# Performance work log

Measured on AMD Instinct MI355X. Metric: run time of the kernel, lower is better.

## Reference

```python
import jax, jax.numpy as jnp
import numpy as np

B, CD, ZL = 512, 64, 16
HID, SE, NC, SL = 512, 512, 9, 64
EPS = 1e-5


def _conv_t1d(x, w, b, stride, opad):
    # torch ConvTranspose1d weight layout: [in, out, k]; pad=0
    k = w.shape[-1]
    w2 = jnp.flip(jnp.transpose(w, (1, 0, 2)), -1)  # [out, in, k]
    y = jax.lax.conv_general_dilated(
        x, w2, window_strides=(1,),
        padding=[(k - 1, k - 1 + opad)], lhs_dilation=(stride,),
        dimension_numbers=('NCH', 'OIH', 'NCH'))
    return y + b[None, :, None]


def _bn(x, g, bt, m, v):  # eval-mode BatchNorm1d over channel dim of [B,C,L]
    return (x - m[None, :, None]) * (g * jax.lax.rsqrt(v + EPS))[None, :, None] + bt[None, :, None]


def _gru(x, h, wih, whh, bih, bhh):  # torch GRUCell gate order r,z,n
    gi = x @ wih.T + bih
    gh = h @ whh.T + bhh
    ir, iz, inn = jnp.split(gi, 3, axis=-1)
    hr, hz, hn = jnp.split(gh, 3, axis=-1)
    r = jax.nn.sigmoid(ir + hr)
    z = jax.nn.sigmoid(iz + hz)
    n = jnp.tanh(inn + r * hn)
    return (1.0 - z) * n + z * h


def setup_inputs() -> dict:
    ks = jax.random.split(jax.random.key(0), 24)
    s = 0.05
    H2 = HID // 2
    in1 = H2 + 2 * NC
    d = {}
    d['quantized_z'] = jax.random.normal(ks[0], (B, CD, ZL), jnp.float32)
    d['note_target'] = (jax.random.uniform(ks[1], (B, SL, NC)) > 0.5).astype(jnp.float32)
    d['skel'] = (jax.random.uniform(ks[2], (B, SL, NC)) > 0.5).astype(jnp.float32)
    d['skel_encoded'] = jax.random.normal(ks[3], (B, SE), jnp.float32)
    d['training'] = 0
    d['teacher_forcing_ratio'] = 0
    d['ct1_w'] = jax.random.normal(ks[4], (CD, HID, 4)) * s
    d['ct1_b'] = jnp.zeros((HID,))
    d['bn1_g'] = jnp.ones((HID,))
    d['bn1_b'] = jnp.zeros((HID,))
    d['bn1_m'] = jax.random.normal(ks[5], (HID,)) * 0.1
    d['bn1_v'] = 1.0 + 0.1 * jax.random.uniform(ks[6], (HID,))
    d['ct2_w'] = jax.random.normal(ks[7], (HID, H2, 4)) * s
    d['ct2_b'] = jnp.zeros((H2,))
    d['bn2_g'] = jnp.ones((H2,))
    d['bn2_b'] = jnp.zeros((H2,))
    d['bn2_m'] = jax.random.normal(ks[8], (H2,)) * 0.1
    d['bn2_v'] = 1.0 + 0.1 * jax.random.uniform(ks[9], (H2,))
    d['hfc_w'] = jax.random.normal(ks[10], (HID, SE)) * s
    d['hfc_b'] = jnp.zeros((HID,))
    d['gru1_wih'] = jax.random.normal(ks[11], (3 * HID, in1)) * s
    d['gru1_whh'] = jax.random.normal(ks[12], (3 * HID, HID)) * s
    d['gru1_bih'] = jnp.zeros((3 * HID,))
    d['gru1_bhh'] = jnp.zeros((3 * HID,))
    d['gru2_wih'] = jax.random.normal(ks[13], (3 * HID, HID)) * s
    d['gru2_whh'] = jax.random.normal(ks[14], (3 * HID, HID)) * s
    d['gru2_bih'] = jnp.zeros((3 * HID,))
    d['gru2_bhh'] = jnp.zeros((3 * HID,))
    d['nfc_w'] = jax.random.normal(ks[15], (NC, HID)) * s
    d['nfc_b'] = jnp.zeros((NC,))
    return d


def _forward(quantized_z, skel, skel_encoded,
             ct1_w, ct1_b, bn1_g, bn1_b, bn1_m, bn1_v,
             ct2_w, ct2_b, bn2_g, bn2_b, bn2_m, bn2_v,
             hfc_w, hfc_b,
             gru1_wih, gru1_whh, gru1_bih, gru1_bhh,
             gru2_wih, gru2_whh, gru2_bih, gru2_bhh,
             nfc_w, nfc_b):
    lrelu = lambda x: jax.nn.leaky_relu(x, 0.2)
    y = lrelu(_bn(_conv_t1d(quantized_z, ct1_w, ct1_b, 2, 1), bn1_g, bn1_b, bn1_m, bn1_v))
    y = lrelu(_bn(_conv_t1d(y, ct2_w, ct2_b, 2, 0), bn2_g, bn2_b, bn2_m, bn2_v))
    inputs = jnp.transpose(y, (0, 2, 1))[:, :SL]  # [B, SL, HID//2]
    h1_0 = skel_encoded @ hfc_w.T + hfc_b          # [B, HID]
    keys = jax.random.split(jax.random.key(42), SL)

    def step(carry, xs):
        h1, h2, out = carry
        i, x_in, x_sk, k = xs
        cat = jnp.concatenate([out, x_in, x_sk], axis=-1)  # [B, NC + HID//2 + NC]
        h1 = _gru(cat, h1, gru1_wih, gru1_whh, gru1_bih, gru1_bhh)
        h2 = jnp.where(i == 0, h1, h2)  # hx[1] = hx[0] at first step
        h2 = _gru(h1, h2, gru2_wih, gru2_whh, gru2_bih, gru2_bhh)
        logits = h2 @ nfc_w.T + nfc_b
        r = jax.random.uniform(k, logits.shape, logits.dtype)
        out = (jax.nn.sigmoid(logits) - r > 0).astype(logits.dtype)  # eval-mode Bernoulli sampling
        return (h1, h2, out), logits

    carry0 = (h1_0, jnp.zeros_like(h1_0), jnp.zeros((quantized_z.shape[0], NC), h1_0.dtype))
    xs = (jnp.arange(SL), jnp.transpose(inputs, (1, 0, 2)), jnp.transpose(skel, (1, 0, 2)), keys)
    _, logits = jax.lax.scan(step, carry0, xs)
    return jnp.transpose(logits, (1, 0, 2))  # [B, SL, NC]


def reference(quantized_z, note_target, skel, skel_encoded, training, teacher_forcing_ratio,
              ct1_w, ct1_b, bn1_g, bn1_b, bn1_m, bn1_v,
              ct2_w, ct2_b, bn2_g, bn2_b, bn2_m, bn2_v,
              hfc_w, hfc_b,
              gru1_wih, gru1_whh, gru1_bih, gru1_bhh,
              gru2_wih, gru2_whh, gru2_bih, gru2_bhh,
              nfc_w, nfc_b):
    # training=0 (eval): dropout is identity, BN uses running stats, always sample feedback.
    # note_target / teacher_forcing_ratio are unused on the eval path.
    return _forward(quantized_z, skel, skel_encoded,
                    ct1_w, ct1_b, bn1_g, bn1_b, bn1_m, bn1_v,
                    ct2_w, ct2_b, bn2_g, bn2_b, bn2_m, bn2_v,
                    hfc_w, hfc_b,
                    gru1_wih, gru1_whh, gru1_bih, gru1_bhh,
                    gru2_wih, gru2_whh, gru2_bih, gru2_bhh,
                    nfc_w, nfc_b)
```

## Files before the change

### kernel.cpp

```cpp
#include <hip/hip_runtime.h>
#include <stdint.h>

typedef uint32_t u32; typedef uint16_t u16; typedef unsigned long long u64;
typedef __attribute__((ext_vector_type(8))) short short8;
typedef __attribute__((ext_vector_type(4))) float f32x4;

#define DEV static __device__ __forceinline__
#define MFMA16 __builtin_amdgcn_mfma_f32_16x16x32_bf16

#define BATCH 512
#define CD    64
#define ZL    16
#define HID   512
#define H2D   256
#define NC    9
#define SLEN  64
#define L1    35

#define JAX_PARTITIONABLE 1

#define P_W      2850816
#define WOFF_SKH 4276224
#define WOFF_HPL 4538368
#define WOFF_HF  6111232
#define WOFF_LOG 7159808
#define WOFF_FLG 7684096
#define WOFF_XH  9175040

template<int V> struct IC { static constexpr int value = V; };

DEV float bf2f(u16 h){ u32 u = ((u32)h) << 16; float f; __builtin_memcpy(&f,&u,4); return f; }
DEV u16 f2bf(float f){ u32 u; __builtin_memcpy(&u,&f,4); return (u16)((u + 0x7FFFu + ((u>>16)&1u)) >> 16); }

DEV float ldf(const float* p){ return __hip_atomic_load(p, __ATOMIC_RELAXED, __HIP_MEMORY_SCOPE_AGENT); }
DEV u32 ldu32(const u32* p){ return __hip_atomic_load(p, __ATOMIC_RELAXED, __HIP_MEMORY_SCOPE_AGENT); }
DEV u64 ldu64(const u64* p){ return __hip_atomic_load(p, __ATOMIC_RELAXED, __HIP_MEMORY_SCOPE_AGENT); }
DEV void stu32(u32* p, u32 v){ __hip_atomic_store(p, v, __ATOMIC_RELAXED, __HIP_MEMORY_SCOPE_AGENT); }

DEV void threefry2x32(u32 k0, u32 k1, u32 x0, u32 x1, u32 &o0, u32 &o1){
  const u32 ks2 = k0 ^ k1 ^ 0x1BD11BDAu;
#define TF_R(d) { x0 += x1; x1 = (x1 << (d)) | (x1 >> (32 - (d))); x1 ^= x0; }
  x0 += k0; x1 += k1;
  TF_R(13) TF_R(15) TF_R(26) TF_R(6)
  x0 += k1;  x1 += ks2 + 1u;
  TF_R(17) TF_R(29) TF_R(16) TF_R(24)
  x0 += ks2; x1 += k0 + 2u;
  TF_R(13) TF_R(15) TF_R(26) TF_R(6)
  x0 += k0;  x1 += k1 + 3u;
  TF_R(17) TF_R(29) TF_R(16) TF_R(24)
  x0 += k1;  x1 += ks2 + 4u;
  TF_R(13) TF_R(15) TF_R(26) TF_R(6)
  x0 += ks2; x1 += k0 + 5u;
#undef TF_R
  o0 = x0; o1 = x1;
}
DEV void step_key(int t, u32 &ka, u32 &kb){
#if JAX_PARTITIONABLE
  threefry2x32(0u, 42u, 0u, (u32)t, ka, kb);
#else
  u32 j0 = 2u*(u32)t, j1 = j0 + 1u, a0, a1;
  if (j0 < 64u){ threefry2x32(0u,42u, j0, 64u+j0, a0, a1); ka = a0; }
  else         { threefry2x32(0u,42u, j0-64u, j0, a0, a1); ka = a1; }
  if (j1 < 64u){ threefry2x32(0u,42u, j1, 64u+j1, a0, a1); kb = a0; }
  else         { threefry2x32(0u,42u, j1-64u, j1, a0, a1); kb = a1; }
#endif
}
DEV float rng_uniform(u32 ka, u32 kb, u32 f){
  u32 bits, o0, o1;
#if JAX_PARTITIONABLE
  threefry2x32(ka, kb, 0u, f, o0, o1);
  bits = o0 ^ o1;
#else
  const u32 HALF = (u32)(BATCH*NC/2);
  if (f < HALF){ threefry2x32(ka, kb, f, f+HALF, o0, o1); bits = o0; }
  else         { threefry2x32(ka, kb, f-HALF, f, o0, o1); bits = o1; }
#endif
  u32 fb = (bits >> 9) | 0x3F800000u;
  float fv; __builtin_memcpy(&fv,&fb,4);
  return fv - 1.0f;
}

__global__ __launch_bounds__(256) void k_conv1(
    const float* __restrict__ z, const float* __restrict__ w1, const float* __restrict__ b1,
    const float* __restrict__ g1, const float* __restrict__ bt1, const float* __restrict__ m1,
    const float* __restrict__ v1, float* __restrict__ y1out)
{
  int t = blockIdx.x, bg = blockIdx.y*8, tid = threadIdx.x;
  __shared__ float zsh[2][8][CD];
  int k0 = t & 1, sA = (t-k0)>>1, sB = sA-1;
  bool vA = (sA>=0 && sA<ZL), vB = (sB>=0 && sB<ZL);
  for (int l = tid; l < 2*8*CD; l += 256){
    int p = l>>9, bb = (l>>6)&7, i = l&63;
    int s = p ? sB : sA; bool v = p ? vB : vA;
    zsh[p][bb][i] = v ? z[((bg+bb)*CD+i)*ZL + s] : 0.f;
  }
  __syncthreads();
  const float4* w1v = (const float4*)w1;
  for (int o = tid; o < HID; o += 256){
    float acc[8] = {0,0,0,0,0,0,0,0};
    for (int i = 0; i < CD; i++){
      float4 wv = w1v[i*HID + o];
      float wA = k0 ? wv.y : wv.x, wB = k0 ? wv.w : wv.z;
      #pragma unroll
      for (int bb = 0; bb < 8; bb++) acc[bb] += zsh[0][bb][i]*wA + zsh[1][bb][i]*wB;
    }
    float xb = b1[o], sc = g1[o]/sqrtf(v1[o]+1e-5f), mm = m1[o], be = bt1[o];
    #pragma unroll
    for (int bb = 0; bb < 8; bb++){
      float y = (acc[bb]+xb-mm)*sc + be;
      y = (y>0.f)? y : 0.2f*y;
      y1out[((bg+bb)*L1 + t)*HID + o] = y;
    }
  }
}

__global__ __launch_bounds__(256) void k_conv2(
    const float* __restrict__ y1, const float* __restrict__ w2, const float* __restrict__ b2,
    const float* __restrict__ g2, const float* __restrict__ bt2, const float* __restrict__ m2,
    const float* __restrict__ v2, u16* __restrict__ xh, u16* __restrict__ xl)
{
  int t = blockIdx.x, bg = blockIdx.y*8, tid = threadIdx.x;
  __shared__ float ysh[2][8][HID];
  int k0 = t & 1, sA = (t-k0)>>1, sB = sA-1;
  bool vB = (sB >= 0);
  for (int l = tid; l < 2*8*HID; l += 256){
    int p = l>>12, bb = (l>>9)&7, o = l&511;
    int s = p ? sB : sA; bool v = p ? vB : true;
    ysh[p][bb][o] = v ? y1[((bg+bb)*L1 + s)*HID + o] : 0.f;
  }
  __syncthreads();
  int c = tid;
  float acc[8] = {0,0,0,0,0,0,0,0};
  const float4* w2v = (const float4*)w2;
  for (int o4 = 0; o4 < HID; o4 += 4){
    float wA[4], wB[4];
    #pragma unroll
    for (int j = 0; j < 4; j++){
      float4 wv = w2v[(o4+j)*H2D + c];
      wA[j] = k0 ? wv.y : wv.x; wB[j] = k0 ? wv.w : wv.z;
    }
    #pragma unroll
    for (int bb = 0; bb < 8; bb++){
      const float4 ya = *(const float4*)&ysh[0][bb][o4];
      const float4 yb = *(const float4*)&ysh[1][bb][o4];
      acc[bb] += ya.x*wA[0]+ya.y*wA[1]+ya.z*wA[2]+ya.w*wA[3]
               + yb.x*wB[0]+yb.y*wB[1]+yb.z*wB[2]+yb.w*wB[3];
    }
  }
  float xb = b2[c], sc = g2[c]/sqrtf(v2[c]+1e-5f), mm = m2[c], be = bt2[c];
  #pragma unroll
  for (int bb = 0; bb < 8; bb++){
    float y = (acc[bb]+xb-mm)*sc + be;
    y = (y>0.f)? y : 0.2f*y;
    u16 hi = f2bf(y); u16 lo = f2bf(y - bf2f(hi));
    size_t o = ((size_t)t*512 + bg + bb)*256 + c;
    xh[o] = hi; xl[o] = lo;
  }
}

__global__ __launch_bounds__(256) void k_prep(
    const float* __restrict__ wih1, const float* __restrict__ whh1,
    const float* __restrict__ wih2, const float* __restrict__ whh2,
    const float* __restrict__ skel, float* __restrict__ ws)
{
  u16* wp = (u16*)ws;
  u16* skh = (u16*)(ws + WOFF_SKH);
  float* logacc = ws + WOFF_LOG;
  u32* flg = (u32*)(ws + WOFF_FLG);
  int stride = gridDim.x*256, i0 = blockIdx.x*256 + threadIdx.x;
  for (int i = i0; i < P_W; i += stride){
    int r = i; float v;
    if (r < 491520){
      int n = r/320, k = r - n*320; v = 0.f;
      if (k < 256)      v = wih1[(size_t)n*274 + 9 + k];
      else if (k < 265) v = wih1[(size_t)n*274 + 265 + (k-256)];
      else if (k < 274) v = wih1[(size_t)n*274 + (k-265)];
    }
    else if (r < 1277952){ int rr = r-491520;  int n = rr>>9, k = rr&511; v = whh1[((size_t)n<<9)+k]; }
    else if (r < 2064384){ int rr = r-1277952; int n = rr>>9, k = rr&511; v = wih2[((size_t)n<<9)+k]; }
    else                 { int rr = r-2064384; int n = rr>>9, k = rr&511; v = whh2[((size_t)n<<9)+k]; }
    u16 l0 = f2bf(v);
    float r1 = v - bf2f(l0); u16 l1 = f2bf(r1);
    float r2 = r1 - bf2f(l1); u16 l2 = f2bf(r2);
    wp[i] = l0; wp[P_W + i] = l1; wp[2*P_W + i] = l2;
  }
  for (int i = i0; i < 524288; i += stride){
    int c = i & 15, r = i >> 4, b = r & 511, tt = r >> 9;
    float v = (c < 9) ? skel[((size_t)b*64 + tt)*9 + c] : 0.f;
    skh[i] = f2bf(v);
  }
  for (int i = i0; i < 524288; i += stride) logacc[i] = 0.f;
  for (int i = i0; i < 512; i += stride) flg[i] = 0u;
}

__global__ __launch_bounds__(256) void k_h0(
    const float* __restrict__ se, const float* __restrict__ w, const float* __restrict__ bias,
    float* __restrict__ ws)
{
  float* h1af = ws + WOFF_HF;
  u16* hpl = (u16*)(ws + WOFF_HPL);
  int b = blockIdx.x, tid = threadIdx.x;
  __shared__ float ssh[HID];
  for (int i = tid; i < HID; i += 256) ssh[i] = se[b*HID + i];
  __syncthreads();
  for (int j = tid; j < HID; j += 256){
    float acc = 0.f;
    for (int q = 0; q < HID; q++) acc += ssh[q]*w[j*HID + q];
    float v = acc + bias[j];
    h1af[(size_t)b*512 + j] = v;
    u16 l0 = f2bf(v);
    float r1 = v - bf2f(l0); u16 l1 = f2bf(r1);
    float r2 = r1 - bf2f(l1); u16 l2 = f2bf(r2);
    hpl[(size_t)b*512 + j] = l0;
    hpl[262144 + (size_t)b*512 + j] = l1;
    hpl[524288 + (size_t)b*512 + j] = l2;
  }
}

__global__ __launch_bounds__(768, 1) void k_persist(
    float* __restrict__ ws,
    const float* __restrict__ bih1, const float* __restrict__ bhh1,
    const float* __restrict__ bih2, const float* __restrict__ bhh2,
    const float* __restrict__ nfw,  const float* __restrict__ nfb,
    float* __restrict__ dout)
{
  const int tid = threadIdx.x;
  const int wvid = __builtin_amdgcn_readfirstlane(tid >> 6);
  const int g  = wvid >> 2;
  const int mh = (wvid >> 1) & 1;
  const int jn = wvid & 1;
  const int lane = tid & 63;
  const int mloc = lane & 15;
  const int q8 = (lane >> 4) * 8;
  const int q4 = (lane >> 4) * 4;
  const int bg = blockIdx.x & 15;
  const int nstrip = blockIdx.x >> 4;
  const int b0 = bg * 32;
  const int n0 = nstrip * 32;

  u16* wp = (u16*)ws;
  const u16* skh = (const u16*)(ws + WOFF_SKH);
  u16* hpl = (u16*)(ws + WOFF_HPL);
  const float* h1af = ws + WOFF_HF;
  float* logacc = ws + WOFF_LOG;
  u32* flgH = (u32*)(ws + WOFF_FLG);
  u32* flgL = flgH + 256;
  const u16* xh = (const u16*)(ws + WOFF_XH);
  const u16* xl = xh + 8388608;

  __shared__ __align__(16) u16 Abuf[2][3][32][72];
  __shared__ __align__(16) u16 Wbuf[2][3][3][32][72];
  __shared__ __align__(16) float eg[4][32][33];
  __shared__ __align__(16) float h2loc[32][33];
  __shared__ __align__(16) u16 out_sh[32][12];

  int t = 0;
  float2 hp1 = {0.f,0.f}, hp2 = {0.f,0.f};

  if (tid < 384) ((u16*)out_sh)[tid] = 0;
  if (tid < 512){
    int bi = tid >> 4, nl2 = (tid & 15)*2;
    hp1.x = h1af[(size_t)(b0+bi)*512 + n0 + nl2];
    hp1.y = h1af[(size_t)(b0+bi)*512 + n0 + nl2 + 1];
  }

  auto soft_bar = [&](){
    __builtin_amdgcn_sched_barrier(0);
    asm volatile("s_waitcnt lgkmcnt(0)" ::: "memory");
    __builtin_amdgcn_s_barrier();
    __builtin_amdgcn_sched_barrier(0);
  };
  auto arrive = [&](u32* f, u32 tok){
    __syncthreads();
    if (tid == 0) __hip_atomic_store(&f[bg*16 + nstrip], tok, __ATOMIC_RELEASE, __HIP_MEMORY_SCOPE_AGENT);
  };
  auto waitbar = [&](u32* f, u32 tok){
    if (tid < 16) while (ldu32(&f[bg*16 + tid]) < tok) __builtin_amdgcn_s_sleep(2);
    __syncthreads();
  };

  auto run_phase = [&](auto mc, auto nwc, int Kp, size_t SUB, const u16* hb, f32x4 &acc){
    constexpr int MODE = decltype(mc)::value;
    constexpr int NW = decltype(nwc)::value;
    short8 RwA[3], RwB[3];
    u64 RaA[2], RaB[2];

    auto loadW = [&](short8 (&R)[3], int kc){
      #pragma unroll
      for (int i = 0; i < 3; i++){
        int idx = tid + i*768;
        int gp = idx >> 8, r = idx & 255, nn = r >> 3, ck = r & 7;
        const u16* src = wp + (size_t)(gp % 3)*P_W + SUB
                       + ((size_t)((gp/3)*512 + n0 + nn))*(size_t)Kp + kc + ck*8;
        R[i] = *(const short8*)src;
      }
    };
    auto writeW = [&](int buf, short8 (&R)[3]){
      #pragma unroll
      for (int i = 0; i < 3; i++){
        int idx = tid + i*768;
        int gp = idx >> 8, r = idx & 255, nn = r >> 3, ck = r & 7;
        *(short8*)&Wbuf[buf][gp/3][gp%3][nn][ck*8] = R[i];
      }
    };
    auto loadA = [&](u64 (&R)[2], int kc){
      int idx = tid;
      if constexpr (MODE == 1){
        int p = idx >> 8, r = idx & 255, bi = r >> 3, ck = r & 7;
        const u16* src = hb + (size_t)p*262144 + (size_t)(b0+bi)*512 + kc + ck*8;
        R[0] = ldu64((const u64*)src);
        R[1] = ldu64((const u64*)(src + 4));
      } else {
        if (idx < 512){
          int p = idx >> 8, r = idx & 255, bi = r >> 3, ck = r & 7;
          if (kc < 256){
            const u64* src = (const u64*)((p ? xl : xh) + ((size_t)t*512 + b0 + bi)*256 + kc + ck*8);
            R[0] = src[0]; R[1] = src[1];
          } else {
            u64 w0 = 0, w1 = 0;
            if (p == 0){
              #pragma unroll
              for (int e2 = 0; e2 < 4; e2++){
                int kg = 256 + ck*8 + e2;
                u16 val = 0;
                if (kg < 265) val = skh[((size_t)t*512 + b0 + bi)*16 + (kg - 256)];
                else if (kg < 274) val = out_sh[bi][kg - 265];
                w0 |= ((u64)val) << (16*e2);
              }
              #pragma unroll
              for (int e2 = 0; e2 < 4; e2++){
                int kg = 260 + ck*8 + e2;
                u16 val = 0;
                if (kg < 265) val = skh[((size_t)t*512 + b0 + bi)*16 + (kg - 256)];
                else if (kg < 274) val = out_sh[bi][kg - 265];
                w1 |= ((u64)val) << (16*e2);
              }
            }
            R[0] = w0; R[1] = w1;
          }
        }
      }
    };
    auto writeA = [&](int buf, u64 (&R)[2]){
      constexpr int NCH = (MODE == 1) ? 768 : 512;
      int idx = tid;
      if (idx < NCH){
        int p = idx >> 8, r = idx & 255, bi = r >> 3, ck = r & 7;
        u64* d = (u64*)&Abuf[buf][p][bi][ck*8];
        d[0] = R[0]; d[1] = R[1];
      }
    };
    auto compute = [&](int buf){
      const int ar = mh*16 + mloc;
      const int wr = jn*16 + mloc;
      #pragma unroll
      for (int ks = 0; ks < 2; ks++){
        const int ko = ks*32 + q8;
        short8 a0 = *(const short8*)&Abuf[buf][0][ar][ko];
        short8 a1 = *(const short8*)&Abuf[buf][1][ar][ko];
        short8 a2 = {};
        if constexpr (MODE == 1) a2 = *(const short8*)&Abuf[buf][2][ar][ko];
        short8 w0 = *(const short8*)&Wbuf[buf][g][0][wr][ko];
        short8 w1 = *(const short8*)&Wbuf[buf][g][1][wr][ko];
        short8 w2 = *(const short8*)&Wbuf[buf][g][2][wr][ko];
        acc = MFMA16(a0, w0, acc, 0, 0, 0);
        acc = MFMA16(a0, w1, acc, 0, 0, 0);
        acc = MFMA16(a1, w0, acc, 0, 0, 0);
        acc = MFMA16(a0, w2, acc, 0, 0, 0);
        if constexpr (MODE == 1) acc = MFMA16(a2, w0, acc, 0, 0, 0);
        acc = MFMA16(a1, w1, acc, 0, 0, 0);
      }
    };

    loadW(RwA, 0); loadA(RaA, 0);
    loadW(RwB, 64); loadA(RaB, 64);
    writeW(0, RwA); writeA(0, RaA);
    soft_bar();

    auto stepw = [&](int w, short8 (&Rl)[3], u64 (&Al)[2], short8 (&Rs)[3], u64 (&As)[2]){
      if (w + 2 < NW){ loadW(Rl, (w+2)*64); loadA(Al, (w+2)*64); }
      compute(w & 1);
      if (w + 1 < NW){ writeW((w+1)&1, Rs); writeA((w+1)&1, As); }
      soft_bar();
    };
    #pragma unroll
    for (int w = 0; w < NW; w += 2){
      stepw(w, RwA, RaA, RwB, RaB);
      if (w + 1 < NW) stepw(w+1, RwB, RaB, RwA, RaA);
    }
  };

  auto epilogue = [&](const float* bih, const float* bhh, u16* hnl,
                      float2 &hp, bool cell2, bool init2,
                      const f32x4 &accI, const f32x4 &accH){
    #pragma unroll
    for (int i2 = 0; i2 < 4; i2++){
      int row = mh*16 + q4 + i2, col = jn*16 + mloc;
      if (g < 2) eg[g][row][col] = accI[i2] + accH[i2];
      else { eg[2][row][col] = accI[i2]; eg[3][row][col] = accH[i2]; }
    }
    __syncthreads();
    if (tid < 512){
      int bi = tid >> 4, nl2 = (tid & 15)*2, b = b0 + bi;
      float hv[2];
      float hpv0 = hp.x, hpv1 = hp.y;
      #pragma unroll
      for (int u = 0; u < 2; u++){
        int nl = nl2 + u, n = n0 + nl;
        float rr = 1.f/(1.f + expf(-(eg[0][bi][nl] + bih[n] + bhh[n])));
        float zz = 1.f/(1.f + expf(-(eg[1][bi][nl] + bih[512+n] + bhh[512+n])));
        float nn2 = tanhf(eg[2][bi][nl] + bih[1024+n] + rr*(eg[3][bi][nl] + bhh[1024+n]));
        float hprev = u ? hpv1 : hpv0;
        hv[u] = (1.f - zz)*nn2 + zz*hprev;
        if (cell2) h2loc[bi][nl] = hv[u];
      }
      hp.x = hv[0]; hp.y = hv[1];
      if (init2){ hp2.x = hv[0]; hp2.y = hv[1]; }
      u16 A0 = f2bf(hv[0]); float ra = hv[0] - bf2f(A0);
      u16 A1 = f2bf(ra);    float ra2 = ra - bf2f(A1);
      u16 A2 = f2bf(ra2);
      u16 B0 = f2bf(hv[1]); float rb = hv[1] - bf2f(B0);
      u16 B1 = f2bf(rb);    float rb2 = rb - bf2f(B1);
      u16 B2 = f2bf(rb2);
      size_t base = (size_t)b*512 + n0 + nl2;
      stu32((u32*)(hnl + base),          (u32)A0 | ((u32)B0 << 16));
      stu32((u32*)(hnl + 262144 + base), (u32)A1 | ((u32)B1 << 16));
      stu32((u32*)(hnl + 524288 + base), (u32)A2 | ((u32)B2 << 16));
    }
    __syncthreads();
    if (cell2){
      for (int e = tid; e < 288; e += 768){
        int c = e % 9, bi = e / 9;
        float s = 0.f;
        #pragma unroll
        for (int nl = 0; nl < 32; nl++) s += nfw[c*512 + n0 + nl]*h2loc[bi][nl];
        atomicAdd(&logacc[((size_t)t*512 + b0 + bi)*16 + c], s);
      }
    }
  };

  auto sample_phase = [&](int tp){
    for (int e = tid; e < 288; e += 768){
      int c = e % 9, bi = e / 9, b = b0 + bi;
      float lg = ldf(&logacc[((size_t)tp*512 + b)*16 + c]) + nfb[c];
      if (nstrip == 0) dout[((size_t)b*64 + tp)*9 + c] = lg;
      if (tp < 63){
        u32 ka, kb; step_key(tp, ka, kb);
        float rr = rng_uniform(ka, kb, (u32)(b*9 + c));
        float sg = 1.f/(1.f + expf(-lg));
        out_sh[bi][c] = (sg - rr > 0.f) ? (u16)0x3F80 : (u16)0;
      }
    }
    __syncthreads();
  };

  for (t = 0; t < 64; t++){
    const u16* h1pl = hpl + (size_t)((t & 1) ? 1 : 0)*786432;
    u16*       h1nl = hpl + (size_t)((t & 1) ? 0 : 1)*786432;
    const u16* h2pl = hpl + (size_t)((t & 1) ? 2 : 3)*786432;
    u16*       h2nl = hpl + (size_t)((t & 1) ? 3 : 2)*786432;

    f32x4 accI = {0,0,0,0}, accH = {0,0,0,0};
    run_phase(IC<1>{}, IC<8>{}, 512, (size_t)491520, h1pl, accH);
    if (t > 0){ waitbar(flgL, (u32)t); sample_phase(t-1); }
    run_phase(IC<0>{}, IC<5>{}, 320, (size_t)0, nullptr, accI);
    epilogue(bih1, bhh1, h1nl, hp1, false, (t == 0), accI, accH);
    arrive(flgH, (u32)(t+1));

    f32x4 accI2 = {0,0,0,0}, accH2 = {0,0,0,0};
    if (t == 0){
      waitbar(flgH, 1u);
      run_phase(IC<1>{}, IC<8>{}, 512, (size_t)2064384, h1nl, accH2);
    } else {
      run_phase(IC<1>{}, IC<8>{}, 512, (size_t)2064384, h2pl, accH2);
      waitbar(flgH, (u32)(t+1));
    }
    run_phase(IC<1>{}, IC<8>{}, 512, (size_t)1277952, h1nl, accI2);
    epilogue(bih2, bhh2, h2nl, hp2, true, false, accI2, accH2);
    arrive(flgL, (u32)(t+1));
  }
  waitbar(flgL, 64u);
  sample_phase(63);
}

extern "C" void kernel_launch(void* const* d_in, const int* in_sizes, int n_in,
                              void* d_out, int out_size, void* d_ws, size_t ws_size,
                              hipStream_t stream) {
  (void)in_sizes; (void)n_in; (void)out_size; (void)ws_size;
  const float* z       = (const float*)d_in[0];
  const float* skel    = (const float*)d_in[2];
  const float* se      = (const float*)d_in[3];
  const float* ct1_w   = (const float*)d_in[6];
  const float* ct1_b   = (const float*)d_in[7];
  const float* bn1_g   = (const float*)d_in[8];
  const float* bn1_b   = (const float*)d_in[9];
  const float* bn1_m   = (const float*)d_in[10];
  const float* bn1_v   = (const float*)d_in[11];
  const float* ct2_w   = (const float*)d_in[12];
  const float* ct2_b   = (const float*)d_in[13];
  const float* bn2_g   = (const float*)d_in[14];
  const float* bn2_b   = (const float*)d_in[15];
  const float* bn2_m   = (const float*)d_in[16];
  const float* bn2_v   = (const float*)d_in[17];
  const float* hfc_w   = (const float*)d_in[18];
  const float* hfc_b   = (const float*)d_in[19];
  const float* g1_wih  = (const float*)d_in[20];
  const float* g1_whh  = (const float*)d_in[21];
  const float* g1_bih  = (const float*)d_in[22];
  const float* g1_bhh  = (const float*)d_in[23];
  const float* g2_wih  = (const float*)d_in[24];
  const float* g2_whh  = (const float*)d_in[25];
  const float* g2_bih  = (const float*)d_in[26];
  const float* g2_bhh  = (const float*)d_in[27];
  const float* nfc_w   = (const float*)d_in[28];
  const float* nfc_b   = (const float*)d_in[29];

  float* ws = (float*)d_ws;
  float* y1 = ws;
  u16* xh = (u16*)(ws + WOFF_XH);
  u16* xl = xh + 8388608;
  float* dout = (float*)d_out;

  k_conv1<<<dim3(L1, BATCH/8), 256, 0, stream>>>(z, ct1_w, ct1_b, bn1_g, bn1_b, bn1_m, bn1_v, y1);
  k_conv2<<<dim3(SLEN, BATCH/8), 256, 0, stream>>>(y1, ct2_w, ct2_b, bn2_g, bn2_b, bn2_m, bn2_v, xh, xl);
  k_prep<<<4096, 256, 0, stream>>>(g1_wih, g1_whh, g2_wih, g2_whh, skel, ws);
  k_h0<<<BATCH, 256, 0, stream>>>(se, hfc_w, hfc_b, ws);

  void* args[] = {
    (void*)&ws, (void*)&g1_bih, (void*)&g1_bhh, (void*)&g2_bih, (void*)&g2_bhh,
    (void*)&nfc_w, (void*)&nfc_b, (void*)&dout
  };
  hipLaunchCooperativeKernel((const void*)k_persist, dim3(256), dim3(768), args, 0, stream);
}
```

Before: 3.770 ms.

## Switch GRU matmuls to 32x32 MFMA with split-K across waves

Each gate group's 32x32 output tile is now computed by four waves, each using 32x32x16 bf16 MFMA over a separate K-slice, instead of four 16x16 sub-tiles with 16x16x32 MFMA. The partial sums are written to shared memory and reduced in the epilogue, and that scratch area is aliased onto the weight buffer to save LDS. The aim is fewer MFMA issues and LDS reads per wave, traded for larger accumulators (more VGPRs) and a four-way reduction in the epilogue. Reusing the weight buffer for the partials relies on every wave having finished compute before the epilogue writes.

Measured after the change: 3.993 ms. +5.9%, slower.

```diff
diff --git a/kernel.cpp b/kernel.cpp
--- a/kernel.cpp
+++ b/kernel.cpp
@@ -3,10 +3,10 @@
 
 typedef uint32_t u32; typedef uint16_t u16; typedef unsigned long long u64;
 typedef __attribute__((ext_vector_type(8))) short short8;
-typedef __attribute__((ext_vector_type(4))) float f32x4;
+typedef __attribute__((ext_vector_type(16))) float f32x16;
 
 #define DEV static __device__ __forceinline__
-#define MFMA16 __builtin_amdgcn_mfma_f32_16x16x32_bf16
+#define MFMA32 __builtin_amdgcn_mfma_f32_32x32x16_bf16
 
 #define BATCH 512
 #define CD    64
@@ -227,12 +227,10 @@
   const int tid = threadIdx.x;
   const int wvid = __builtin_amdgcn_readfirstlane(tid >> 6);
   const int g  = wvid >> 2;
-  const int mh = (wvid >> 1) & 1;
-  const int jn = wvid & 1;
+  const int ks = wvid & 3;
   const int lane = tid & 63;
-  const int mloc = lane & 15;
-  const int q8 = (lane >> 4) * 8;
-  const int q4 = (lane >> 4) * 4;
+  const int wn = lane & 31;
+  const int kq = lane >> 5;
   const int bg = blockIdx.x & 15;
   const int nstrip = blockIdx.x >> 4;
   const int b0 = bg * 32;
@@ -248,11 +246,11 @@
   const u16* xh = (const u16*)(ws + WOFF_XH);
   const u16* xl = xh + 8388608;
 
+  __shared__ __align__(16) u16 Wbuf[2][3][3][32][72];
   __shared__ __align__(16) u16 Abuf[2][3][32][72];
-  __shared__ __align__(16) u16 Wbuf[2][3][3][32][72];
-  __shared__ __align__(16) float eg[4][32][33];
   __shared__ __align__(16) float h2loc[32][33];
   __shared__ __align__(16) u16 out_sh[32][12];
+  auto eg = (float (*)[4][32][33])(void*)&Wbuf[0][0][0][0][0];
 
   int t = 0;
   float2 hp1 = {0.f,0.f}, hp2 = {0.f,0.f};
@@ -279,7 +277,7 @@
     __syncthreads();
   };
 
-  auto run_phase = [&](auto mc, auto nwc, int Kp, size_t SUB, const u16* hb, f32x4 &acc){
+  auto run_phase = [&](auto mc, auto nwc, int Kp, size_t SUB, const u16* hb, f32x16 &acc){
     constexpr int MODE = decltype(mc)::value;
     constexpr int NW = decltype(nwc)::value;
     short8 RwA[3], RwB[3];
@@ -351,25 +349,20 @@
       }
     };
     auto compute = [&](int buf){
-      const int ar = mh*16 + mloc;
-      const int wr = jn*16 + mloc;
-      #pragma unroll
-      for (int ks = 0; ks < 2; ks++){
-        const int ko = ks*32 + q8;
-        short8 a0 = *(const short8*)&Abuf[buf][0][ar][ko];
-        short8 a1 = *(const short8*)&Abuf[buf][1][ar][ko];
-        short8 a2 = {};
-        if constexpr (MODE == 1) a2 = *(const short8*)&Abuf[buf][2][ar][ko];
-        short8 w0 = *(const short8*)&Wbuf[buf][g][0][wr][ko];
-        short8 w1 = *(const short8*)&Wbuf[buf][g][1][wr][ko];
-        short8 w2 = *(const short8*)&Wbuf[buf][g][2][wr][ko];
-        acc = MFMA16(a0, w0, acc, 0, 0, 0);
-        acc = MFMA16(a0, w1, acc, 0, 0, 0);
-        acc = MFMA16(a1, w0, acc, 0, 0, 0);
-        acc = MFMA16(a0, w2, acc, 0, 0, 0);
-        if constexpr (MODE == 1) acc = MFMA16(a2, w0, acc, 0, 0, 0);
-        acc = MFMA16(a1, w1, acc, 0, 0, 0);
-      }
+      const int ko = ks*16 + kq*8;
+      short8 a0 = *(const short8*)&Abuf[buf][0][wn][ko];
+      short8 a1 = *(const short8*)&Abuf[buf][1][wn][ko];
+      short8 a2 = {};
+      if constexpr (MODE == 1) a2 = *(const short8*)&Abuf[buf][2][wn][ko];
+      short8 w0 = *(const short8*)&Wbuf[buf][g][0][wn][ko];
+      short8 w1 = *(const short8*)&Wbuf[buf][g][1][wn][ko];
+      short8 w2 = *(const short8*)&Wbuf[buf][g][2][wn][ko];
+      acc = MFMA32(a0, w0, acc, 0, 0, 0);
+      acc = MFMA32(a0, w1, acc, 0, 0, 0);
+      acc = MFMA32(a1, w0, acc, 0, 0, 0);
+      acc = MFMA32(a0, w2, acc, 0, 0, 0);
+      if constexpr (MODE == 1) acc = MFMA32(a2, w0, acc, 0, 0, 0);
+      acc = MFMA32(a1, w1, acc, 0, 0, 0);
     };
 
     loadW(RwA, 0); loadA(RaA, 0);
@@ -392,12 +385,12 @@
 
   auto epilogue = [&](const float* bih, const float* bhh, u16* hnl,
                       float2 &hp, bool cell2, bool init2,
-                      const f32x4 &accI, const f32x4 &accH){
+                      const f32x16 &accI, const f32x16 &accH){
     #pragma unroll
-    for (int i2 = 0; i2 < 4; i2++){
-      int row = mh*16 + q4 + i2, col = jn*16 + mloc;
-      if (g < 2) eg[g][row][col] = accI[i2] + accH[i2];
-      else { eg[2][row][col] = accI[i2]; eg[3][row][col] = accH[i2]; }
+    for (int r5 = 0; r5 < 16; r5++){
+      int row = (r5 & 3) + 8*(r5 >> 2) + 4*kq;
+      if (g < 2) eg[g][ks][row][wn] = accI[r5] + accH[r5];
+      else { eg[2][ks][row][wn] = accI[r5]; eg[3][ks][row][wn] = accH[r5]; }
     }
     __syncthreads();
     if (tid < 512){
@@ -407,9 +400,13 @@
       #pragma unroll
       for (int u = 0; u < 2; u++){
         int nl = nl2 + u, n = n0 + nl;
-        float rr = 1.f/(1.f + expf(-(eg[0][bi][nl] + bih[n] + bhh[n])));
-        float zz = 1.f/(1.f + expf(-(eg[1][bi][nl] + bih[512+n] + bhh[512+n])));
-        float nn2 = tanhf(eg[2][bi][nl] + bih[1024+n] + rr*(eg[3][bi][nl] + bhh[1024+n]));
+        float rsum = (eg[0][0][bi][nl] + eg[0][1][bi][nl]) + (eg[0][2][bi][nl] + eg[0][3][bi][nl]);
+        float zsum = (eg[1][0][bi][nl] + eg[1][1][bi][nl]) + (eg[1][2][bi][nl] + eg[1][3][bi][nl]);
+        float nih  = (eg[2][0][bi][nl] + eg[2][1][bi][nl]) + (eg[2][2][bi][nl] + eg[2][3][bi][nl]);
+        float nhh  = (eg[3][0][bi][nl] + eg[3][1][bi][nl]) + (eg[3][2][bi][nl] + eg[3][3][bi][nl]);
+        float rr = 1.f/(1.f + expf(-(rsum + bih[n] + bhh[n])));
+        float zz = 1.f/(1.f + expf(-(zsum + bih[512+n] + bhh[512+n])));
+        float nn2 = tanhf(nih + bih[1024+n] + rr*(nhh + bhh[1024+n]));
         float hprev = u ? hpv1 : hpv0;
         hv[u] = (1.f - zz)*nn2 + zz*hprev;
         if (cell2) h2loc[bi][nl] = hv[u];
@@ -460,14 +457,16 @@
     const u16* h2pl = hpl + (size_t)((t & 1) ? 2 : 3)*786432;
     u16*       h2nl = hpl + (size_t)((t & 1) ? 3 : 2)*786432;
 
-    f32x4 accI = {0,0,0,0}, accH = {0,0,0,0};
+    f32x16 accI = {0,0,0,0,0,0,0,0,0,0,0,0,0,0,0,0};
+    f32x16 accH = {0,0,0,0,0,0,0,0,0,0,0,0,0,0,0,0};
     run_phase(IC<1>{}, IC<8>{}, 512, (size_t)491520, h1pl, accH);
     if (t > 0){ waitbar(flgL, (u32)t); sample_phase(t-1); }
     run_phase(IC<0>{}, IC<5>{}, 320, (size_t)0, nullptr, accI);
     epilogue(bih1, bhh1, h1nl, hp1, false, (t == 0), accI, accH);
     arrive(flgH, (u32)(t+1));
 
-    f32x4 accI2 = {0,0,0,0}, accH2 = {0,0,0,0};
+    f32x16 accI2 = {0,0,0,0,0,0,0,0,0,0,0,0,0,0,0,0};
+    f32x16 accH2 = {0,0,0,0,0,0,0,0,0,0,0,0,0,0,0,0};
     if (t == 0){
       waitbar(flgH, 1u);
       run_phase(IC<1>{}, IC<8>{}, 512, (size_t)2064384, h1nl, accH2);
```
